# Optimization experiments

Hardware: AMD Instinct MI355X
Metric: run time of the kernel (lower is better)

Reference implementation:

```python
import jax, jax.numpy as jnp
import numpy as np
from jax import lax

B, T_IN, D = 32, 512, 384
F = 384      # x_predictor_filter_size
K = 3        # kernel, padding=1 -> same length
LN_EPS = 1e-5


def setup_inputs() -> dict:
    key = jax.random.key(0)
    ks = jax.random.split(key, 8)
    s = 0.02
    return {
        "x": jax.random.normal(ks[0], (B, T_IN, D), dtype=jnp.float32),
        "target": jax.random.randint(ks[1], (B, T_IN), 0, 8, dtype=jnp.int32),
        "mel_max_length": 4096,
        "conv1_w": jax.random.normal(ks[2], (F, D, K), dtype=jnp.float32) * s,
        "conv1_b": jnp.zeros((F,), jnp.float32),
        "ln1_g": jnp.ones((F,), jnp.float32),
        "ln1_b": jnp.zeros((F,), jnp.float32),
        "conv2_w": jax.random.normal(ks[3], (F, F, K), dtype=jnp.float32) * s,
        "conv2_b": jnp.zeros((F,), jnp.float32),
        "ln2_g": jnp.ones((F,), jnp.float32),
        "ln2_b": jnp.zeros((F,), jnp.float32),
        "lin_w": jax.random.normal(ks[4], (F, 1), dtype=jnp.float32) * s,
        "lin_b": jnp.zeros((1,), jnp.float32),
    }


def _conv1d_same(h_ncl, w, b):
    # h_ncl: [B, C_in, T], w: [C_out, C_in, K], padding=1
    out = lax.conv_general_dilated(h_ncl, w, window_strides=(1,), padding=[(1, 1)],
                                   dimension_numbers=("NCH", "OIH", "NCH"))
    return out + b[None, :, None]


def _layernorm(h, g, b):
    mu = jnp.mean(h, axis=-1, keepdims=True)
    var = jnp.var(h, axis=-1, keepdims=True)
    return (h - mu) * lax.rsqrt(var + LN_EPS) * g + b


def _duration_predictor(x, conv1_w, conv1_b, ln1_g, ln1_b, conv2_w, conv2_b, ln2_g, ln2_b, lin_w, lin_b):
    h = _conv1d_same(jnp.transpose(x, (0, 2, 1)), conv1_w, conv1_b)       # [B,F,T]
    h = jax.nn.relu(_layernorm(jnp.transpose(h, (0, 2, 1)), ln1_g, ln1_b))  # [B,T,F]
    h = _conv1d_same(jnp.transpose(h, (0, 2, 1)), conv2_w, conv2_b)
    h = jax.nn.relu(_layernorm(jnp.transpose(h, (0, 2, 1)), ln2_g, ln2_b))
    return (h @ lin_w + lin_b)[..., 0]  # [B, T_in]


def _length_regulate(x, target, mel_max_length):
    # Equivalent to alignment @ x with one-hot alignment built by create_alignment,
    # expressed as a duration-indexed gather (same math, no dense [B,Tout,Tin]).
    ends = jnp.cumsum(target, axis=1)                 # [B, T_in]
    m = jnp.arange(mel_max_length)                    # [T_out]
    idx = jax.vmap(lambda e: jnp.searchsorted(e, m, side="right"))(ends)  # [B, T_out]
    valid = idx < target.shape[1]                     # frames past total duration -> zero pad
    idx = jnp.minimum(idx, target.shape[1] - 1)
    out = jnp.take_along_axis(x, idx[:, :, None], axis=1)  # [B, T_out, D]
    return out * valid[:, :, None].astype(x.dtype)


def reference(x, target, mel_max_length, conv1_w, conv1_b, ln1_g, ln1_b,
              conv2_w, conv2_b, ln2_g, ln2_b, lin_w, lin_b):
    dur_pred = _duration_predictor(x, conv1_w, conv1_b, ln1_g, ln1_b,
                                   conv2_w, conv2_b, ln2_g, ln2_b, lin_w, lin_b)
    output = _length_regulate(x, target, mel_max_length)
    return output, dur_pred
```

## Files before the change

kernel.cpp:

```cpp
#include <hip/hip_runtime.h>
#include <cstdint>
#include <cstddef>

#define B_   32
#define TIN  512
#define D_   384
#define F_   384
#define TOUT 4096

typedef __bf16 bf16x8 __attribute__((ext_vector_type(8)));
typedef float  f32x4  __attribute__((ext_vector_type(4)));
typedef unsigned short u16x8 __attribute__((ext_vector_type(8)));

__device__ __forceinline__ unsigned short f2bf(float f) {
  unsigned int u = __float_as_uint(f);
  u += 0x7fff + ((u >> 16) & 1);
  return (unsigned short)(u >> 16);
}

__global__ __launch_bounds__(256) void prep_w(
    const float* __restrict__ w1, const float* __restrict__ w2,
    unsigned short* __restrict__ Wt1, unsigned short* __restrict__ Wt2) {
  int g = blockIdx.x * 256 + threadIdx.x;
  const int FD = F_ * D_;
  int which = g >= FD;
  const float* w = which ? w2 : w1;
  unsigned short* o = which ? Wt2 : Wt1;
  int e = g - which * FD;
  o[e]          = f2bf(w[e * 3 + 0]);
  o[FD + e]     = f2bf(w[e * 3 + 1]);
  o[2 * FD + e] = f2bf(w[e * 3 + 2]);
}

#define NCONV 256
#define NGATH 1024

__global__ __launch_bounds__(512, 4) void fused(
    const unsigned short* __restrict__ Wt1, const unsigned short* __restrict__ Wt2,
    const float* __restrict__ b1, const float* __restrict__ g1, const float* __restrict__ be1,
    const float* __restrict__ b2, const float* __restrict__ g2, const float* __restrict__ be2,
    const float* __restrict__ lw, const float* __restrict__ lb,
    float* __restrict__ dur, const int* __restrict__ target,
    const f32x4* __restrict__ x4, f32x4* __restrict__ out4) {
  __shared__ __attribute__((aligned(16))) char smem[68736];

  const int tid = threadIdx.x;
  const int bx  = blockIdx.x;

  if (bx >= NCONV) {
    int gi = bx - NCONV;
    int* ends  = (int*)smem;
    int* idx_s = (int*)(smem + 2048);
    int b  = gi >> 5;
    int r0 = (gi & 31) * 128;
    ends[tid] = target[b * TIN + tid];
    __syncthreads();
    for (int off = 1; off < 512; off <<= 1) {
      int add = (tid >= off) ? ends[tid - off] : 0;
      __syncthreads();
      ends[tid] += add;
      __syncthreads();
    }
    if (tid < 128) {
      int m = r0 + tid;
      int lo = 0, hi = 512;
      while (lo < hi) {
        int mid = (lo + hi) >> 1;
        if (ends[mid] <= m) lo = mid + 1; else hi = mid;
      }
      idx_s[tid] = (lo < TIN) ? lo : -1;
    }
    __syncthreads();
    const f32x4* xb = x4 + (size_t)b * (TIN * 96);
    f32x4* ob = out4 + ((size_t)b * TOUT + r0) * 96;
    #pragma unroll 4
    for (int it = 0; it < 24; ++it) {
      int j = it * 512 + tid;
      int row = j / 96;
      int c = j - row * 96;
      int id = idx_s[row];
      f32x4 v = {0.f, 0.f, 0.f, 0.f};
      if (id >= 0) v = xb[id * 96 + c];
      __builtin_nontemporal_store(v, ob + j);
    }
    return;
  }

  char* As = smem;
  float* stats  = (float*)(smem + 62976);
  float* stats2 = (float*)(smem + 68096);

  const int wave = tid >> 6;
  const int lane = tid & 63;
  const int quad = lane >> 4;
  const int l15  = lane & 15;
  const int wn   = wave * 48;
  const int m0   = bx * 64;
  const int b    = m0 >> 9;
  const int t0   = m0 & 511;

  for (int p = 0; p < 7; ++p) {
    int ch = p * 512 + tid;
    if (ch < 3264) {
      int row = ch / 48;
      int ci  = ch - row * 48;
      int t   = t0 - 2 + row;
      u16x8 val;
      if ((unsigned)t >= (unsigned)TIN) {
        val = (u16x8)0;
      } else {
        const f32x4* xr = x4 + ((size_t)(b * TIN + t)) * 96 + ci * 2;
        f32x4 v0 = xr[0], v1 = xr[1];
        val[0] = f2bf(v0[0]); val[1] = f2bf(v0[1]); val[2] = f2bf(v0[2]); val[3] = f2bf(v0[3]);
        val[4] = f2bf(v1[0]); val[5] = f2bf(v1[1]); val[6] = f2bf(v1[2]); val[7] = f2bf(v1[3]);
      }
      unsigned int byte = ((unsigned int)(row * 768 + ci * 16)) ^ (((unsigned)row & 7u) << 4);
      *(u16x8*)(As + byte) = val;
    }
  }
  __syncthreads();

  f32x4 acc[5][3];
  for (int i = 0; i < 5; ++i)
    for (int j = 0; j < 3; ++j)
      acc[i][j] = (f32x4){0.f, 0.f, 0.f, 0.f};

  {
    const unsigned short* Bb = Wt1 + (size_t)(wn + l15) * D_ + quad * 8;
    bf16x8 bvn[3];
    for (int ni = 0; ni < 3; ++ni)
      bvn[ni] = *(const bf16x8*)(Bb + ni * (16 * D_));
    #pragma unroll 1
    for (int kc = 0; kc < 36; ++kc) {
      bf16x8 bv[3];
      bv[0] = bvn[0]; bv[1] = bvn[1]; bv[2] = bvn[2];
      if (kc < 35) {
        int kn = kc + 1;
        int kw2 = kn / 12, d02 = (kn - kw2 * 12) * 32;
        const unsigned short* Bk = Bb + (size_t)kw2 * (F_ * D_) + d02;
        for (int ni = 0; ni < 3; ++ni)
          bvn[ni] = *(const bf16x8*)(Bk + ni * (16 * D_));
      }
      int kw = kc / 12, d0 = (kc - kw * 12) * 32;
      int rb = l15 + kw;
      unsigned int sw = (((unsigned)rb) & 7u) << 4;
      unsigned int base = (unsigned int)(rb * 768 + d0 * 2 + quad * 16);
      bf16x8 av[5];
      for (int mi = 0; mi < 5; ++mi)
        av[mi] = *(const bf16x8*)(As + ((base + mi * 12288) ^ sw));
      for (int mi = 0; mi < 5; ++mi)
        for (int ni = 0; ni < 3; ++ni)
          acc[mi][ni] = __builtin_amdgcn_mfma_f32_16x16x32_bf16(av[mi], bv[ni], acc[mi][ni], 0, 0, 0);
    }
  }

  {
    float g1v[3], be1v[3], bb1[3];
    for (int ni = 0; ni < 3; ++ni) {
      int c = wn + ni * 16 + l15;
      g1v[ni] = g1[c]; be1v[ni] = be1[c]; bb1[ni] = b1[c];
    }
    for (int mi = 0; mi < 5; ++mi)
      for (int r = 0; r < 4; ++r) {
        float s = 0.f, ssq = 0.f;
        for (int ni = 0; ni < 3; ++ni) {
          float y = acc[mi][ni][r] + bb1[ni];
          s += y; ssq += y * y;
        }
        for (int off = 1; off < 16; off <<= 1) {
          s   += __shfl_xor(s, off);
          ssq += __shfl_xor(ssq, off);
        }
        if (l15 == 0) {
          int row = mi * 16 + quad * 4 + r;
          stats[(row * 8 + wave) * 2 + 0] = s;
          stats[(row * 8 + wave) * 2 + 1] = ssq;
        }
      }
    __syncthreads();
    if (tid < 80) {
      float s = 0.f, ssq = 0.f;
      for (int w = 0; w < 8; ++w) {
        s   += stats[(tid * 8 + w) * 2 + 0];
        ssq += stats[(tid * 8 + w) * 2 + 1];
      }
      float mean = s * (1.f / 384.f);
      float var  = ssq * (1.f / 384.f) - mean * mean;
      stats2[tid * 2 + 0] = mean;
      stats2[tid * 2 + 1] = rsqrtf(var + 1e-5f);
    }
    __syncthreads();
    for (int mi = 0; mi < 5; ++mi)
      for (int r = 0; r < 4; ++r) {
        int row = mi * 16 + quad * 4 + r;
        if (row < 66) {
          float mean = stats2[row * 2 + 0];
          float rstd = stats2[row * 2 + 1];
          int th = t0 - 1 + row;
          bool valid = (unsigned)th < (unsigned)TIN;
          unsigned int hb = (((unsigned)row) & 7u) << 4;
          for (int ni = 0; ni < 3; ++ni) {
            float y = (acc[mi][ni][r] + bb1[ni] - mean) * rstd * g1v[ni] + be1v[ni];
            y = y > 0.f ? y : 0.f;
            if (!valid) y = 0.f;
            unsigned int byte = ((unsigned int)(row * 768 + (wn + ni * 16 + l15) * 2)) ^ hb;
            *(unsigned short*)(As + byte) = f2bf(y);
          }
        }
      }
    __syncthreads();
  }

  f32x4 acc2[4][3];
  for (int i = 0; i < 4; ++i)
    for (int j = 0; j < 3; ++j)
      acc2[i][j] = (f32x4){0.f, 0.f, 0.f, 0.f};

  {
    const unsigned short* Bb = Wt2 + (size_t)(wn + l15) * D_ + quad * 8;
    bf16x8 bvn[3];
    for (int ni = 0; ni < 3; ++ni)
      bvn[ni] = *(const bf16x8*)(Bb + ni * (16 * D_));
    #pragma unroll 1
    for (int kc = 0; kc < 36; ++kc) {
      bf16x8 bv[3];
      bv[0] = bvn[0]; bv[1] = bvn[1]; bv[2] = bvn[2];
      if (kc < 35) {
        int kn = kc + 1;
        int kw2 = kn / 12, d02 = (kn - kw2 * 12) * 32;
        const unsigned short* Bk = Bb + (size_t)kw2 * (F_ * D_) + d02;
        for (int ni = 0; ni < 3; ++ni)
          bvn[ni] = *(const bf16x8*)(Bk + ni * (16 * D_));
      }
      int kw = kc / 12, d0 = (kc - kw * 12) * 32;
      int rb = l15 + kw;
      unsigned int sw = (((unsigned)rb) & 7u) << 4;
      unsigned int base = (unsigned int)(rb * 768 + d0 * 2 + quad * 16);
      bf16x8 av[4];
      for (int mi = 0; mi < 4; ++mi)
        av[mi] = *(const bf16x8*)(As + ((base + mi * 12288) ^ sw));
      for (int mi = 0; mi < 4; ++mi)
        for (int ni = 0; ni < 3; ++ni)
          acc2[mi][ni] = __builtin_amdgcn_mfma_f32_16x16x32_bf16(av[mi], bv[ni], acc2[mi][ni], 0, 0, 0);
    }
  }

  {
    float g2v[3], be2v[3], lwv[3], bb2[3];
    for (int ni = 0; ni < 3; ++ni) {
      int c = wn + ni * 16 + l15;
      g2v[ni] = g2[c]; be2v[ni] = be2[c]; lwv[ni] = lw[c]; bb2[ni] = b2[c];
    }
    for (int mi = 0; mi < 4; ++mi)
      for (int r = 0; r < 4; ++r) {
        float s = 0.f, ssq = 0.f;
        for (int ni = 0; ni < 3; ++ni) {
          float y = acc2[mi][ni][r] + bb2[ni];
          s += y; ssq += y * y;
        }
        for (int off = 1; off < 16; off <<= 1) {
          s   += __shfl_xor(s, off);
          ssq += __shfl_xor(ssq, off);
        }
        if (l15 == 0) {
          int row = mi * 16 + quad * 4 + r;
          stats[(row * 8 + wave) * 2 + 0] = s;
          stats[(row * 8 + wave) * 2 + 1] = ssq;
        }
      }
    __syncthreads();
    if (tid < 64) {
      float s = 0.f, ssq = 0.f;
      for (int w = 0; w < 8; ++w) {
        s   += stats[(tid * 8 + w) * 2 + 0];
        ssq += stats[(tid * 8 + w) * 2 + 1];
      }
      float mean = s * (1.f / 384.f);
      float var  = ssq * (1.f / 384.f) - mean * mean;
      stats2[tid * 2 + 0] = mean;
      stats2[tid * 2 + 1] = rsqrtf(var + 1e-5f);
    }
    __syncthreads();
    for (int mi = 0; mi < 4; ++mi)
      for (int r = 0; r < 4; ++r) {
        int row = mi * 16 + quad * 4 + r;
        float mean = stats2[row * 2 + 0];
        float rstd = stats2[row * 2 + 1];
        float a = 0.f;
        for (int ni = 0; ni < 3; ++ni) {
          float y = (acc2[mi][ni][r] + bb2[ni] - mean) * rstd * g2v[ni] + be2v[ni];
          y = y > 0.f ? y : 0.f;
          a += y * lwv[ni];
        }
        for (int off = 1; off < 16; off <<= 1) a += __shfl_xor(a, off);
        if (l15 == 0) stats[(row * 8 + wave) * 2 + 0] = a;
      }
    __syncthreads();
    if (tid < 64) {
      float a = 0.f;
      for (int w = 0; w < 8; ++w) a += stats[(tid * 8 + w) * 2 + 0];
      dur[m0 + tid] = a + lb[0];
    }
  }
}

extern "C" void kernel_launch(void* const* d_in, const int* in_sizes, int n_in,
                              void* d_out, int out_size, void* d_ws, size_t ws_size,
                              hipStream_t stream) {
  const float* x      = (const float*)d_in[0];
  const int*   target = (const int*)d_in[1];
  const float* w1  = (const float*)d_in[3];
  const float* b1  = (const float*)d_in[4];
  const float* g1  = (const float*)d_in[5];
  const float* be1 = (const float*)d_in[6];
  const float* w2  = (const float*)d_in[7];
  const float* b2  = (const float*)d_in[8];
  const float* g2  = (const float*)d_in[9];
  const float* be2 = (const float*)d_in[10];
  const float* lw  = (const float*)d_in[11];
  const float* lb  = (const float*)d_in[12];

  float* out = (float*)d_out;
  float* dur = out + (size_t)B_ * TOUT * D_;

  char* ws = (char*)d_ws;
  unsigned short* Wt1 = (unsigned short*)(ws);
  unsigned short* Wt2 = (unsigned short*)(ws + 884736);

  prep_w<<<dim3(1152), dim3(256), 0, stream>>>(w1, w2, Wt1, Wt2);
  fused<<<dim3(NCONV + NGATH), dim3(512), 0, stream>>>(
      Wt1, Wt2, b1, g1, be1, b2, g2, be2, lw, lb,
      dur, target, (const f32x4*)x, (f32x4*)out);
}
```

Before: 283.5 us.

## Halve conv tile to 32 rows, use wave-shuffle scan, nontemporal gather loads

Each conv block now covers 32 time steps instead of 64, which doubles the conv block count to 512. It also cuts shared memory from about 68KB to about 31KB, so more blocks can be resident per CU. The fix-up for the halo row is redundant compute: 36 rows are padded into a 48-row MFMA tile with clamped loads, against 66 rows padded to 80 before. The length-regulator prefix sum now uses wave shuffles plus a per-wave sum, replacing the 9-step shared-memory scan with barriers. Gather reads of x are now nontemporal loads. The costs are a larger halo overhead fraction and more weight re-reads from L2 per output row.

```diff
diff --git a/kernel.cpp b/kernel.cpp
--- a/kernel.cpp
+++ b/kernel.cpp
@@ -32,7 +32,7 @@
   o[2 * FD + e] = f2bf(w[e * 3 + 2]);
 }
 
-#define NCONV 256
+#define NCONV 512
 #define NGATH 1024
 
 __global__ __launch_bounds__(512, 4) void fused(
@@ -42,7 +42,7 @@
     const float* __restrict__ lw, const float* __restrict__ lb,
     float* __restrict__ dur, const int* __restrict__ target,
     const f32x4* __restrict__ x4, f32x4* __restrict__ out4) {
-  __shared__ __attribute__((aligned(16))) char smem[68736];
+  __shared__ __attribute__((aligned(16))) char smem[31104];
 
   const int tid = threadIdx.x;
   const int bx  = blockIdx.x;
@@ -50,17 +50,22 @@
   if (bx >= NCONV) {
     int gi = bx - NCONV;
     int* ends  = (int*)smem;
-    int* idx_s = (int*)(smem + 2048);
+    int* wsum  = (int*)(smem + 2048);
+    int* idx_s = (int*)(smem + 2080);
     int b  = gi >> 5;
     int r0 = (gi & 31) * 128;
-    ends[tid] = target[b * TIN + tid];
-    __syncthreads();
-    for (int off = 1; off < 512; off <<= 1) {
-      int add = (tid >= off) ? ends[tid - off] : 0;
-      __syncthreads();
-      ends[tid] += add;
-      __syncthreads();
-    }
+    int lane = tid & 63, wave = tid >> 6;
+    int v = target[b * TIN + tid];
+    for (int off = 1; off < 64; off <<= 1) {
+      int t = __shfl_up(v, off);
+      if (lane >= off) v += t;
+    }
+    if (lane == 63) wsum[wave] = v;
+    __syncthreads();
+    int base = 0;
+    for (int w = 0; w < 8; ++w) base += (w < wave) ? wsum[w] : 0;
+    ends[tid] = v + base;
+    __syncthreads();
     if (tid < 128) {
       int m = r0 + tid;
       int lo = 0, hi = 512;
@@ -79,29 +84,29 @@
       int row = j / 96;
       int c = j - row * 96;
       int id = idx_s[row];
-      f32x4 v = {0.f, 0.f, 0.f, 0.f};
-      if (id >= 0) v = xb[id * 96 + c];
-      __builtin_nontemporal_store(v, ob + j);
+      f32x4 v4 = {0.f, 0.f, 0.f, 0.f};
+      if (id >= 0) v4 = __builtin_nontemporal_load(xb + id * 96 + c);
+      __builtin_nontemporal_store(v4, ob + j);
     }
     return;
   }
 
   char* As = smem;
-  float* stats  = (float*)(smem + 62976);
-  float* stats2 = (float*)(smem + 68096);
+  float* stats  = (float*)(smem + 27648);
+  float* stats2 = (float*)(smem + 30720);
 
   const int wave = tid >> 6;
   const int lane = tid & 63;
   const int quad = lane >> 4;
   const int l15  = lane & 15;
   const int wn   = wave * 48;
-  const int m0   = bx * 64;
+  const int m0   = bx * 32;
   const int b    = m0 >> 9;
   const int t0   = m0 & 511;
 
-  for (int p = 0; p < 7; ++p) {
+  for (int p = 0; p < 4; ++p) {
     int ch = p * 512 + tid;
-    if (ch < 3264) {
+    if (ch < 1728) {
       int row = ch / 48;
       int ci  = ch - row * 48;
       int t   = t0 - 2 + row;
@@ -120,8 +125,8 @@
   }
   __syncthreads();
 
-  f32x4 acc[5][3];
-  for (int i = 0; i < 5; ++i)
+  f32x4 acc[3][3];
+  for (int i = 0; i < 3; ++i)
     for (int j = 0; j < 3; ++j)
       acc[i][j] = (f32x4){0.f, 0.f, 0.f, 0.f};
 
@@ -142,13 +147,15 @@
           bvn[ni] = *(const bf16x8*)(Bk + ni * (16 * D_));
       }
       int kw = kc / 12, d0 = (kc - kw * 12) * 32;
-      int rb = l15 + kw;
-      unsigned int sw = (((unsigned)rb) & 7u) << 4;
-      unsigned int base = (unsigned int)(rb * 768 + d0 * 2 + quad * 16);
-      bf16x8 av[5];
-      for (int mi = 0; mi < 5; ++mi)
-        av[mi] = *(const bf16x8*)(As + ((base + mi * 12288) ^ sw));
-      for (int mi = 0; mi < 5; ++mi)
+      unsigned int rb = (unsigned)(l15 + kw);
+      unsigned int sw = (rb & 7u) << 4;
+      unsigned int co = (unsigned)(d0 * 2 + quad * 16);
+      bf16x8 av[3];
+      av[0] = *(const bf16x8*)(As + ((rb * 768 + co) ^ sw));
+      av[1] = *(const bf16x8*)(As + (((rb + 16) * 768 + co) ^ sw));
+      unsigned int r2 = rb + 32; if (r2 > 35u) r2 = 35u;
+      av[2] = *(const bf16x8*)(As + ((r2 * 768 + co) ^ sw));
+      for (int mi = 0; mi < 3; ++mi)
         for (int ni = 0; ni < 3; ++ni)
           acc[mi][ni] = __builtin_amdgcn_mfma_f32_16x16x32_bf16(av[mi], bv[ni], acc[mi][ni], 0, 0, 0);
     }
@@ -160,7 +167,7 @@
       int c = wn + ni * 16 + l15;
       g1v[ni] = g1[c]; be1v[ni] = be1[c]; bb1[ni] = b1[c];
     }
-    for (int mi = 0; mi < 5; ++mi)
+    for (int mi = 0; mi < 3; ++mi)
       for (int r = 0; r < 4; ++r) {
         float s = 0.f, ssq = 0.f;
         for (int ni = 0; ni < 3; ++ni) {
@@ -178,7 +185,7 @@
         }
       }
     __syncthreads();
-    if (tid < 80) {
+    if (tid < 48) {
       float s = 0.f, ssq = 0.f;
       for (int w = 0; w < 8; ++w) {
         s   += stats[(tid * 8 + w) * 2 + 0];
@@ -190,10 +197,10 @@
       stats2[tid * 2 + 1] = rsqrtf(var + 1e-5f);
     }
     __syncthreads();
-    for (int mi = 0; mi < 5; ++mi)
+    for (int mi = 0; mi < 3; ++mi)
       for (int r = 0; r < 4; ++r) {
         int row = mi * 16 + quad * 4 + r;
-        if (row < 66) {
+        if (row < 34) {
           float mean = stats2[row * 2 + 0];
           float rstd = stats2[row * 2 + 1];
           int th = t0 - 1 + row;
@@ -211,8 +218,8 @@
     __syncthreads();
   }
 
-  f32x4 acc2[4][3];
-  for (int i = 0; i < 4; ++i)
+  f32x4 acc2[2][3];
+  for (int i = 0; i < 2; ++i)
     for (int j = 0; j < 3; ++j)
       acc2[i][j] = (f32x4){0.f, 0.f, 0.f, 0.f};
 
@@ -233,13 +240,13 @@
           bvn[ni] = *(const bf16x8*)(Bk + ni * (16 * D_));
       }
       int kw = kc / 12, d0 = (kc - kw * 12) * 32;
-      int rb = l15 + kw;
-      unsigned int sw = (((unsigned)rb) & 7u) << 4;
-      unsigned int base = (unsigned int)(rb * 768 + d0 * 2 + quad * 16);
-      bf16x8 av[4];
-      for (int mi = 0; mi < 4; ++mi)
-        av[mi] = *(const bf16x8*)(As + ((base + mi * 12288) ^ sw));
-      for (int mi = 0; mi < 4; ++mi)
+      unsigned int rb = (unsigned)(l15 + kw);
+      unsigned int sw = (rb & 7u) << 4;
+      unsigned int co = (unsigned)(d0 * 2 + quad * 16);
+      bf16x8 av[2];
+      av[0] = *(const bf16x8*)(As + ((rb * 768 + co) ^ sw));
+      av[1] = *(const bf16x8*)(As + (((rb + 16) * 768 + co) ^ sw));
+      for (int mi = 0; mi < 2; ++mi)
         for (int ni = 0; ni < 3; ++ni)
           acc2[mi][ni] = __builtin_amdgcn_mfma_f32_16x16x32_bf16(av[mi], bv[ni], acc2[mi][ni], 0, 0, 0);
     }
@@ -251,7 +258,7 @@
       int c = wn + ni * 16 + l15;
       g2v[ni] = g2[c]; be2v[ni] = be2[c]; lwv[ni] = lw[c]; bb2[ni] = b2[c];
     }
-    for (int mi = 0; mi < 4; ++mi)
+    for (int mi = 0; mi < 2; ++mi)
       for (int r = 0; r < 4; ++r) {
         float s = 0.f, ssq = 0.f;
         for (int ni = 0; ni < 3; ++ni) {
@@ -269,7 +276,7 @@
         }
       }
     __syncthreads();
-    if (tid < 64) {
+    if (tid < 32) {
       float s = 0.f, ssq = 0.f;
       for (int w = 0; w < 8; ++w) {
         s   += stats[(tid * 8 + w) * 2 + 0];
@@ -281,7 +288,7 @@
       stats2[tid * 2 + 1] = rsqrtf(var + 1e-5f);
     }
     __syncthreads();
-    for (int mi = 0; mi < 4; ++mi)
+    for (int mi = 0; mi < 2; ++mi)
       for (int r = 0; r < 4; ++r) {
         int row = mi * 16 + quad * 4 + r;
         float mean = stats2[row * 2 + 0];
@@ -296,7 +303,7 @@
         if (l15 == 0) stats[(row * 8 + wave) * 2 + 0] = a;
       }
     __syncthreads();
-    if (tid < 64) {
+    if (tid < 32) {
       float a = 0.f;
       for (int w = 0; w < 8; ++w) a += stats[(tid * 8 + w) * 2 + 0];
       dur[m0 + tid] = a + lb[0];
```

Result: slower. 366.9 us (+29.4%).

## Move length-regulate gather into weight-prep kernel and split conv into own launch

Applied to the files above, without the earlier changes.

The gather blocks leave the fused conv kernel and join the weight-conversion kernel. They now use 256 threads over 64 output rows, with a two-element-per-thread scan. The conv kernel becomes a standalone 256-block launch, so the gather no longer competes for 512-thread, heavy-LDS slots. The gather now runs serially before the conv instead of overlapping with it, which removes overlap between the memory-bound gather and the compute-bound conv.

```diff
diff --git a/kernel.cpp b/kernel.cpp
--- a/kernel.cpp
+++ b/kernel.cpp
@@ -18,50 +18,37 @@
   return (unsigned short)(u >> 16);
 }
 
-__global__ __launch_bounds__(256) void prep_w(
+#define GB 2048
+
+__global__ __launch_bounds__(256) void gather_prep(
     const float* __restrict__ w1, const float* __restrict__ w2,
-    unsigned short* __restrict__ Wt1, unsigned short* __restrict__ Wt2) {
-  int g = blockIdx.x * 256 + threadIdx.x;
-  const int FD = F_ * D_;
-  int which = g >= FD;
-  const float* w = which ? w2 : w1;
-  unsigned short* o = which ? Wt2 : Wt1;
-  int e = g - which * FD;
-  o[e]          = f2bf(w[e * 3 + 0]);
-  o[FD + e]     = f2bf(w[e * 3 + 1]);
-  o[2 * FD + e] = f2bf(w[e * 3 + 2]);
-}
-
-#define NCONV 256
-#define NGATH 1024
-
-__global__ __launch_bounds__(512, 4) void fused(
-    const unsigned short* __restrict__ Wt1, const unsigned short* __restrict__ Wt2,
-    const float* __restrict__ b1, const float* __restrict__ g1, const float* __restrict__ be1,
-    const float* __restrict__ b2, const float* __restrict__ g2, const float* __restrict__ be2,
-    const float* __restrict__ lw, const float* __restrict__ lb,
-    float* __restrict__ dur, const int* __restrict__ target,
+    unsigned short* __restrict__ Wt1, unsigned short* __restrict__ Wt2,
+    const int* __restrict__ target,
     const f32x4* __restrict__ x4, f32x4* __restrict__ out4) {
-  __shared__ __attribute__((aligned(16))) char smem[68736];
-
-  const int tid = threadIdx.x;
-  const int bx  = blockIdx.x;
-
-  if (bx >= NCONV) {
-    int gi = bx - NCONV;
-    int* ends  = (int*)smem;
-    int* idx_s = (int*)(smem + 2048);
-    int b  = gi >> 5;
-    int r0 = (gi & 31) * 128;
-    ends[tid] = target[b * TIN + tid];
-    __syncthreads();
-    for (int off = 1; off < 512; off <<= 1) {
-      int add = (tid >= off) ? ends[tid - off] : 0;
+  int bx = blockIdx.x;
+  int tid = threadIdx.x;
+
+  if (bx < GB) {
+    __shared__ int ends[512];
+    __shared__ int ps[256];
+    __shared__ int idx_s[64];
+    int b  = bx >> 6;
+    int r0 = (bx & 63) * 64;
+    int a0 = target[b * TIN + 2 * tid];
+    int a1 = target[b * TIN + 2 * tid + 1];
+    ps[tid] = a0 + a1;
+    __syncthreads();
+    for (int off = 1; off < 256; off <<= 1) {
+      int add = (tid >= off) ? ps[tid - off] : 0;
       __syncthreads();
-      ends[tid] += add;
+      ps[tid] += add;
       __syncthreads();
     }
-    if (tid < 128) {
+    int incl = ps[tid];
+    ends[2 * tid + 1] = incl;
+    ends[2 * tid]     = incl - a1;
+    __syncthreads();
+    if (tid < 64) {
       int m = r0 + tid;
       int lo = 0, hi = 512;
       while (lo < hi) {
@@ -73,9 +60,9 @@
     __syncthreads();
     const f32x4* xb = x4 + (size_t)b * (TIN * 96);
     f32x4* ob = out4 + ((size_t)b * TOUT + r0) * 96;
-    #pragma unroll 4
+    #pragma unroll 8
     for (int it = 0; it < 24; ++it) {
-      int j = it * 512 + tid;
+      int j = it * 256 + tid;
       int row = j / 96;
       int c = j - row * 96;
       int id = idx_s[row];
@@ -85,17 +72,39 @@
     }
     return;
   }
-
+  bx -= GB;
+
+  {
+    int g = bx * 256 + tid;
+    const int FD = F_ * D_;
+    int which = g >= FD;
+    const float* w = which ? w2 : w1;
+    unsigned short* o = which ? Wt2 : Wt1;
+    int e = g - which * FD;
+    o[e]          = f2bf(w[e * 3 + 0]);
+    o[FD + e]     = f2bf(w[e * 3 + 1]);
+    o[2 * FD + e] = f2bf(w[e * 3 + 2]);
+  }
+}
+
+__global__ __launch_bounds__(512, 4) void conv(
+    const unsigned short* __restrict__ Wt1, const unsigned short* __restrict__ Wt2,
+    const float* __restrict__ b1, const float* __restrict__ g1, const float* __restrict__ be1,
+    const float* __restrict__ b2, const float* __restrict__ g2, const float* __restrict__ be2,
+    const float* __restrict__ lw, const float* __restrict__ lb,
+    float* __restrict__ dur, const f32x4* __restrict__ x4) {
+  __shared__ __attribute__((aligned(16))) char smem[68736];
   char* As = smem;
   float* stats  = (float*)(smem + 62976);
   float* stats2 = (float*)(smem + 68096);
 
+  const int tid = threadIdx.x;
   const int wave = tid >> 6;
   const int lane = tid & 63;
   const int quad = lane >> 4;
   const int l15  = lane & 15;
   const int wn   = wave * 48;
-  const int m0   = bx * 64;
+  const int m0   = blockIdx.x * 64;
   const int b    = m0 >> 9;
   const int t0   = m0 & 511;
 
@@ -327,8 +336,8 @@
   unsigned short* Wt1 = (unsigned short*)(ws);
   unsigned short* Wt2 = (unsigned short*)(ws + 884736);
 
-  prep_w<<<dim3(1152), dim3(256), 0, stream>>>(w1, w2, Wt1, Wt2);
-  fused<<<dim3(NCONV + NGATH), dim3(512), 0, stream>>>(
-      Wt1, Wt2, b1, g1, be1, b2, g2, be2, lw, lb,
-      dur, target, (const f32x4*)x, (f32x4*)out);
+  gather_prep<<<dim3(GB + 1152), dim3(256), 0, stream>>>(
+      w1, w2, Wt1, Wt2, target, (const f32x4*)x, (f32x4*)out);
+  conv<<<dim3(256), dim3(512), 0, stream>>>(
+      Wt1, Wt2, b1, g1, be1, b2, g2, be2, lw, lb, dur, (const f32x4*)x);
 }
```

Result: slower. 332.5 us (+17.3%).
